# Kernel tuning notes

Measured on AMD Instinct MI355X. Metric: run time of the kernel, lower is better.

Reference implementation:

```python
import jax, jax.numpy as jnp
import numpy as np

# Static problem sizes (must match setup_inputs).
B = 4096      # number of events (unique batch_idx values)
NPER = 2000   # hits per event; NPER == maxhits -> deterministic arange selection
D = 4         # clustering-space dimensionality
EPS = 1e-6


def setup_inputs() -> dict:
    key = jax.random.key(0)
    clust_space = jax.random.normal(key, (B * NPER, D), dtype=jnp.float32)
    # Sorted, equal-sized groups: batch_idx = [0]*NPER, [1]*NPER, ...
    batch_idx = jnp.repeat(jnp.arange(B, dtype=jnp.int32), NPER)
    return {"clust_space": clust_space, "batch_idx": batch_idx}


def reference(clust_space, batch_idx):
    # batch_idx is sorted with equal group sizes, so the per-event Python loop
    # of the original module is a reshape to [B, NPER, D].
    coords = clust_space.reshape(B, NPER, D)
    # Per-event mean and centered coordinates.
    c = coords - coords.mean(axis=1, keepdims=True)            # [B, NPER, D]
    # Covariance: mean over hits of outer products -> [B, D, D] (symmetric).
    cov = jnp.einsum('bnd,bne->bde', c, c) / NPER
    # Symmetric real matrix: eigvalsh == real part of torch.linalg.eig output.
    eig = jnp.linalg.eigvalsh(cov)                             # [B, D]
    pen = jnp.log((eig.mean(axis=-1) / (eig.min(axis=-1) + EPS) - 1.0) ** 2 + 1.0)
    # Original sums the per-event penalties into a scalar loss.
    return pen.sum()
```

## Files before the change

kernel.cpp:

```cpp
#include <hip/hip_runtime.h>
#include <hip/hip_bf16.h>
#include <math.h>

#define NB    4096
#define NPER  2000
#define HALF  1000
#define EPS   1e-6

__global__ __launch_bounds__(256)
void moments_kernel(const float4* __restrict__ cs, float* __restrict__ mom) {
    const int wave = threadIdx.x >> 6;
    const int lane = threadIdx.x & 63;
    const int h = blockIdx.x * 4 + wave;
    const float4* __restrict__ p = cs + (size_t)h * HALF;

    float s0 = 0.f, s1 = 0.f, s2 = 0.f, s3 = 0.f;
    float m00 = 0.f, m01 = 0.f, m02 = 0.f, m03 = 0.f;
    float m11 = 0.f, m12 = 0.f, m13 = 0.f;
    float m22 = 0.f, m23 = 0.f, m33 = 0.f;

#pragma unroll
    for (int i = 0; i < 15; ++i) {
        float4 v = p[i * 64 + lane];
        s0 += v.x; s1 += v.y; s2 += v.z; s3 += v.w;
        m00 += v.x * v.x; m01 += v.x * v.y; m02 += v.x * v.z; m03 += v.x * v.w;
        m11 += v.y * v.y; m12 += v.y * v.z; m13 += v.y * v.w;
        m22 += v.z * v.z; m23 += v.z * v.w;
        m33 += v.w * v.w;
    }
    if (lane < 40) {
        float4 v = p[960 + lane];
        s0 += v.x; s1 += v.y; s2 += v.z; s3 += v.w;
        m00 += v.x * v.x; m01 += v.x * v.y; m02 += v.x * v.z; m03 += v.x * v.w;
        m11 += v.y * v.y; m12 += v.y * v.z; m13 += v.y * v.w;
        m22 += v.z * v.z; m23 += v.z * v.w;
        m33 += v.w * v.w;
    }

    float vals[14] = {s0, s1, s2, s3,
                      m00, m01, m02, m03, m11, m12, m13, m22, m23, m33};
#pragma unroll
    for (int j = 0; j < 14; ++j) {
        float v = vals[j];
#pragma unroll
        for (int off = 32; off > 0; off >>= 1)
            v += __shfl_down(v, off, 64);
        vals[j] = v;
    }

    if (lane == 0) {
        float* o = mom + (size_t)h * 16;
#pragma unroll
        for (int j = 0; j < 14; ++j) o[j] = vals[j];
    }
}

__global__ __launch_bounds__(64)
void pen_kernel(const float* __restrict__ mom, float* __restrict__ out) {
    const int b = blockIdx.x * 64 + threadIdx.x;
    const float* mA = mom + (size_t)(2 * b)     * 16;
    const float* mB = mom + (size_t)(2 * b + 1) * 16;

    double t[14];
#pragma unroll
    for (int j = 0; j < 14; ++j) t[j] = (double)mA[j] + (double)mB[j];

    const double invN = 1.0 / (double)NPER;
    double mu0 = t[0] * invN, mu1 = t[1] * invN,
           mu2 = t[2] * invN, mu3 = t[3] * invN;

    double A[4][4];
    A[0][0] = t[4]  * invN - mu0 * mu0;
    A[0][1] = A[1][0] = t[5]  * invN - mu0 * mu1;
    A[0][2] = A[2][0] = t[6]  * invN - mu0 * mu2;
    A[0][3] = A[3][0] = t[7]  * invN - mu0 * mu3;
    A[1][1] = t[8]  * invN - mu1 * mu1;
    A[1][2] = A[2][1] = t[9]  * invN - mu1 * mu2;
    A[1][3] = A[3][1] = t[10] * invN - mu1 * mu3;
    A[2][2] = t[11] * invN - mu2 * mu2;
    A[2][3] = A[3][2] = t[12] * invN - mu2 * mu3;
    A[3][3] = t[13] * invN - mu3 * mu3;

    for (int sweep = 0; sweep < 8; ++sweep) {
        double off = A[0][1]*A[0][1] + A[0][2]*A[0][2] + A[0][3]*A[0][3]
                   + A[1][2]*A[1][2] + A[1][3]*A[1][3] + A[2][3]*A[2][3];
        if (__all(off < 1e-24)) break;
#pragma unroll
        for (int p = 0; p < 3; ++p) {
#pragma unroll
            for (int q = p + 1; q < 4; ++q) {
                double apq = A[p][q];
                if (fabs(apq) > 1e-300) {
                    double tau = (A[q][q] - A[p][p]) / (2.0 * apq);
                    double tt = (tau >= 0.0 ? 1.0 : -1.0) /
                                (fabs(tau) + sqrt(1.0 + tau * tau));
                    double c = 1.0 / sqrt(1.0 + tt * tt);
                    double s = tt * c;
#pragma unroll
                    for (int k = 0; k < 4; ++k) {
                        double akp = A[k][p], akq = A[k][q];
                        A[k][p] = c * akp - s * akq;
                        A[k][q] = s * akp + c * akq;
                    }
#pragma unroll
                    for (int k = 0; k < 4; ++k) {
                        double apk = A[p][k], aqk = A[q][k];
                        A[p][k] = c * apk - s * aqk;
                        A[q][k] = s * apk + c * aqk;
                    }
                    A[p][q] = 0.0;
                    A[q][p] = 0.0;
                }
            }
        }
    }

    double e0 = A[0][0], e1 = A[1][1], e2 = A[2][2], e3 = A[3][3];
    double mean = 0.25 * (e0 + e1 + e2 + e3);
    double mn = fmin(fmin(e0, e1), fmin(e2, e3));
    double r = mean / (mn + EPS) - 1.0;
    float pen = (float)log(r * r + 1.0);

#pragma unroll
    for (int off = 32; off > 0; off >>= 1)
        pen += __shfl_down(pen, off, 64);
    if (threadIdx.x == 0)
        atomicAdd(out, pen);
}

extern "C" void kernel_launch(void* const* d_in, const int* in_sizes, int n_in,
                              void* d_out, int out_size, void* d_ws, size_t ws_size,
                              hipStream_t stream) {
    const float4* cs = (const float4*)d_in[0];
    float* mom = (float*)d_ws;
    float* out = (float*)d_out;

    hipMemsetAsync(out, 0, sizeof(float), stream);
    moments_kernel<<<2 * NB / 4, 256, 0, stream>>>(cs, mom);
    pen_kernel<<<NB / 64, 64, 0, stream>>>(mom, out);
}
```

Baseline: 211.9 us.

## Use persistent moments grid with batched loads and vectorized moment stores

The moments kernel now launches a fixed grid of 512 workgroups, and each wave loops over four half-events instead of handling one. Inside each half-event the loads are issued in batches of eight and then eight float4s before any accumulation, to raise the number of memory requests in flight per wave. The tail load is made branch-free by masking, and the moment outputs are written as float4 stores. The smaller grid trades launch and scheduling overhead against lower total occupancy and more registers per wave.

New measurement: 211.3 us. Within noise of the previous version (-0.3%).

```diff
diff --git a/kernel.cpp b/kernel.cpp
--- a/kernel.cpp
+++ b/kernel.cpp
@@ -2,56 +2,71 @@
 #include <hip/hip_bf16.h>
 #include <math.h>
 
-#define NB    4096
-#define NPER  2000
-#define HALF  1000
-#define EPS   1e-6
+#define NB     4096
+#define NPER   2000
+#define HALF   1000
+#define HALVES (2 * NB)
+#define WGS    512
+#define WAVES  (WGS * 4)
+#define EPS    1e-6
+
+#define ACC(v)                                                             \
+    do {                                                                   \
+        s0 += (v).x; s1 += (v).y; s2 += (v).z; s3 += (v).w;                \
+        m00 += (v).x * (v).x; m01 += (v).x * (v).y;                        \
+        m02 += (v).x * (v).z; m03 += (v).x * (v).w;                        \
+        m11 += (v).y * (v).y; m12 += (v).y * (v).z; m13 += (v).y * (v).w;  \
+        m22 += (v).z * (v).z; m23 += (v).z * (v).w;                        \
+        m33 += (v).w * (v).w;                                              \
+    } while (0)
 
 __global__ __launch_bounds__(256)
 void moments_kernel(const float4* __restrict__ cs, float* __restrict__ mom) {
     const int wave = threadIdx.x >> 6;
     const int lane = threadIdx.x & 63;
-    const int h = blockIdx.x * 4 + wave;
-    const float4* __restrict__ p = cs + (size_t)h * HALF;
+    const int w0 = blockIdx.x * 4 + wave;
 
-    float s0 = 0.f, s1 = 0.f, s2 = 0.f, s3 = 0.f;
-    float m00 = 0.f, m01 = 0.f, m02 = 0.f, m03 = 0.f;
-    float m11 = 0.f, m12 = 0.f, m13 = 0.f;
-    float m22 = 0.f, m23 = 0.f, m33 = 0.f;
+    for (int e = 0; e < HALVES / WAVES; ++e) {
+        const int h = w0 + e * WAVES;
+        const float4* __restrict__ p = cs + (size_t)h * HALF;
+
+        float s0 = 0.f, s1 = 0.f, s2 = 0.f, s3 = 0.f;
+        float m00 = 0.f, m01 = 0.f, m02 = 0.f, m03 = 0.f;
+        float m11 = 0.f, m12 = 0.f, m13 = 0.f;
+        float m22 = 0.f, m23 = 0.f, m33 = 0.f;
+
+        float4 v[8];
+#pragma unroll
+        for (int r = 0; r < 8; ++r) v[r] = p[r * 64 + lane];
+#pragma unroll
+        for (int r = 0; r < 8; ++r) ACC(v[r]);
 
 #pragma unroll
-    for (int i = 0; i < 15; ++i) {
-        float4 v = p[i * 64 + lane];
-        s0 += v.x; s1 += v.y; s2 += v.z; s3 += v.w;
-        m00 += v.x * v.x; m01 += v.x * v.y; m02 += v.x * v.z; m03 += v.x * v.w;
-        m11 += v.y * v.y; m12 += v.y * v.z; m13 += v.y * v.w;
-        m22 += v.z * v.z; m23 += v.z * v.w;
-        m33 += v.w * v.w;
-    }
-    if (lane < 40) {
-        float4 v = p[960 + lane];
-        s0 += v.x; s1 += v.y; s2 += v.z; s3 += v.w;
-        m00 += v.x * v.x; m01 += v.x * v.y; m02 += v.x * v.z; m03 += v.x * v.w;
-        m11 += v.y * v.y; m12 += v.y * v.z; m13 += v.y * v.w;
-        m22 += v.z * v.z; m23 += v.z * v.w;
-        m33 += v.w * v.w;
-    }
+        for (int r = 0; r < 7; ++r) v[r] = p[512 + r * 64 + lane];
+        float4 vt = p[960 + (lane < 40 ? lane : 0)];
+        if (lane >= 40) { vt.x = 0.f; vt.y = 0.f; vt.z = 0.f; vt.w = 0.f; }
+#pragma unroll
+        for (int r = 0; r < 7; ++r) ACC(v[r]);
+        ACC(vt);
 
-    float vals[14] = {s0, s1, s2, s3,
-                      m00, m01, m02, m03, m11, m12, m13, m22, m23, m33};
+        float vals[14] = {s0, s1, s2, s3,
+                          m00, m01, m02, m03, m11, m12, m13, m22, m23, m33};
 #pragma unroll
-    for (int j = 0; j < 14; ++j) {
-        float v = vals[j];
+        for (int j = 0; j < 14; ++j) {
+            float x = vals[j];
 #pragma unroll
-        for (int off = 32; off > 0; off >>= 1)
-            v += __shfl_down(v, off, 64);
-        vals[j] = v;
-    }
+            for (int off = 32; off > 0; off >>= 1)
+                x += __shfl_down(x, off, 64);
+            vals[j] = x;
+        }
 
-    if (lane == 0) {
-        float* o = mom + (size_t)h * 16;
-#pragma unroll
-        for (int j = 0; j < 14; ++j) o[j] = vals[j];
+        if (lane == 0) {
+            float4* o = (float4*)(mom + (size_t)h * 16);
+            o[0] = make_float4(vals[0], vals[1], vals[2],  vals[3]);
+            o[1] = make_float4(vals[4], vals[5], vals[6],  vals[7]);
+            o[2] = make_float4(vals[8], vals[9], vals[10], vals[11]);
+            o[3] = make_float4(vals[12], vals[13], 0.f, 0.f);
+        }
     }
 }
 
@@ -136,6 +151,6 @@
     float* out = (float*)d_out;
 
     hipMemsetAsync(out, 0, sizeof(float), stream);
-    moments_kernel<<<2 * NB / 4, 256, 0, stream>>>(cs, mom);
+    moments_kernel<<<WGS, 256, 0, stream>>>(cs, mom);
     pen_kernel<<<NB / 64, 64, 0, stream>>>(mom, out);
 }
```
